# Performance work log

Measured on AMD Instinct MI355X. Metric: run time of the kernel, lower is better.

Reference implementation:

```python
import jax, jax.numpy as jnp
import numpy as np

LMAX, MMAX = 6, 2
C, COUT = 64, 64
E = 50000


def _perms():
    # l-primary coefficient order: for l in 0..lmax, m in -min(l,mmax)..min(l,mmax)
    lp = [(l, m) for l in range(LMAX + 1) for m in range(-min(l, MMAX), min(l, MMAX) + 1)]
    # m-primary order: m=0 block, then for each m>0: real (+m) block then imag (-m) block
    mp = [(l, 0) for l in range(LMAX + 1)]
    for m in range(1, MMAX + 1):
        mp += [(l, m) for l in range(m, LMAX + 1)]
        mp += [(l, -m) for l in range(m, LMAX + 1)]
    to_m = np.array([lp.index(p) for p in mp])   # gather: l-primary -> m-primary
    from_m = np.argsort(to_m)                    # inverse gather: m-primary -> l-primary
    return to_m, from_m

TO_M, FROM_M = _perms()


def setup_inputs() -> dict:
    key = jax.random.key(0)
    ks = jax.random.split(key, 6)
    sz0 = LMAX + 1                      # m_size[0] = 7
    in0 = sz0 * C                       # fc_m0 in_features = 448
    out0 = COUT * sz0                   # fc_m0 out_features = 448
    sz1, sz2 = LMAX, LMAX - 1           # m_size[1]=6, m_size[2]=5
    inp = {
        "x_embedding": jax.random.normal(ks[0], (E, len(TO_M), C), dtype=jnp.float32),
        "x_edge": jax.random.normal(ks[1], (E, 1), dtype=jnp.float32),
        "W0": jax.random.normal(ks[2], (out0, in0), dtype=jnp.float32) / np.sqrt(in0),
        "b0": jnp.zeros((out0,), dtype=jnp.float32),
        "W1": jax.random.normal(ks[3], (2 * COUT * sz1, sz1 * C), dtype=jnp.float32) / np.sqrt(2 * sz1 * C),
        "W2": jax.random.normal(ks[4], (2 * COUT * sz2, sz2 * C), dtype=jnp.float32) / np.sqrt(2 * sz2 * C),
    }
    return inp


def reference(x_embedding, x_edge, W0, b0, W1, W2):
    num_edges = x_embedding.shape[0]
    # _m_primary: permute coefficients to m-primary layout
    x = x_embedding[:, TO_M, :]                         # [E, 29, C]
    out = []
    # m = 0 path (fc_m0 with bias)
    sz0 = LMAX + 1
    x0 = x[:, :sz0, :].reshape(num_edges, sz0 * C)
    x0 = x0 @ W0.T + b0                                 # [E, sz0*COUT]
    out.append(x0.reshape(num_edges, sz0, COUT))
    # m = 1..mmax: SO2_m_Convolution (complex multiply structure)
    offset = sz0
    for m, Wm in zip(range(1, MMAX + 1), (W1, W2)):
        sz = LMAX - m + 1
        xm = x[:, offset:offset + 2 * sz, :].reshape(num_edges, 2, sz * C)
        y = jnp.einsum('enk,ok->eno', xm, Wm)           # [E, 2, 2*sz*COUT]
        half = sz * COUT
        x_r, x_i = y[..., :half], y[..., half:]
        x_m_r = x_r[:, 0:1] - x_i[:, 1:2]
        x_m_i = x_r[:, 1:2] + x_i[:, 0:1]
        xm_out = jnp.concatenate((x_m_r, x_m_i), axis=1)  # [E, 2, sz*COUT]
        out.append(xm_out.reshape(num_edges, 2 * sz, COUT))
        offset += 2 * sz
    out = jnp.concatenate(out, axis=1)                  # [E, 29, COUT] m-primary
    # _l_primary: back to l-primary layout
    return out[:, FROM_M, :]
```

## Files before the change

kernel.cpp:

```cpp
#include <hip/hip_runtime.h>
#include <hip/hip_bf16.h>

typedef __attribute__((ext_vector_type(8))) short short8;
typedef __attribute__((ext_vector_type(4))) float f32x4;
typedef __attribute__((ext_vector_type(4))) unsigned int uint4v;

#define NROW 29
#define CCH 64
#define XSTRIDE 1856
#define N0SQ (448*448)
#define N1SQ (768*768)
#define N2SQ (640*640)

__constant__ int d_TO_M[29] = {0,2,6,11,16,21,26, 3,7,12,17,22,27, 1,5,10,15,20,25,
                               8,13,18,23,28, 4,9,14,19,24};

__device__ __forceinline__ short f2bf(float f) {
    __hip_bfloat16 h = __float2bfloat16(f);
    return __builtin_bit_cast(short, h);
}

__global__ __launch_bounds__(256) void prep_weights(const float* __restrict__ W0,
                                                    const float* __restrict__ W1,
                                                    const float* __restrict__ W2,
                                                    short* __restrict__ ws) {
    int idx = blockIdx.x * 256 + threadIdx.x;
    if (idx < N0SQ) {
        ws[idx] = f2bf(W0[idx]);
        return;
    }
    idx -= N0SQ;
    if (idx < N1SQ) {
        int n = idx / 768, k = idx % 768;
        int no = n / 384, ni = n % 384;
        int ko = k / 384, ki = k % 384;
        float v;
        if (no == ko)      v =  W1[ni * 384 + ki];
        else if (no == 0)  v = -W1[(384 + ni) * 384 + ki];
        else               v =  W1[(384 + ni) * 384 + ki];
        ws[N0SQ + idx] = f2bf(v);
        return;
    }
    idx -= N1SQ;
    if (idx < N2SQ) {
        int n = idx / 640, k = idx % 640;
        int no = n / 320, ni = n % 320;
        int ko = k / 320, ki = k % 320;
        float v;
        if (no == ko)      v =  W2[ni * 320 + ki];
        else if (no == 0)  v = -W2[(320 + ni) * 320 + ki];
        else               v =  W2[(320 + ni) * 320 + ki];
        ws[N0SQ + N1SQ + idx] = f2bf(v);
    }
}

#define LDS_STRIDE 72

__global__ __launch_bounds__(256) void so2_gemm(const float* __restrict__ x,
                                                const float* __restrict__ b0,
                                                const short* __restrict__ wsW,
                                                float* __restrict__ out,
                                                int E, int nwg) {
    int orig = blockIdx.x;
    int q = nwg >> 3, r = nwg & 7;
    int xcd = orig & 7, pos = orig >> 3;
    int wgid = (xcd < r ? xcd * (q + 1) : r * (q + 1) + (xcd - r) * q) + pos;

    int etile = wgid / 15;
    int ncol  = wgid % 15;

    int blk, ntl;
    if (ncol < 4)       { blk = 0; ntl = ncol; }
    else if (ncol < 10) { blk = 1; ntl = ncol - 4; }
    else                { blk = 2; ntl = ncol - 10; }
    const int Kb     = (blk == 0) ? 448 : (blk == 1) ? 768 : 640;
    const int ksteps = Kb >> 6;
    const int kbase  = (blk == 0) ? 0 : (blk == 1) ? 7 : 19;
    const int nrows  = (blk == 0) ? 7 : (blk == 1) ? 12 : 10;
    const long woff  = (blk == 0) ? 0 : (blk == 1) ? (long)N0SQ : (long)(N0SQ + N1SQ);
    const short* Wb  = wsW + woff;

    __shared__ short Alds[128 * LDS_STRIDE];
    __shared__ short Blds[128 * LDS_STRIDE];

    const int tid  = threadIdx.x;
    const int w    = tid >> 6, lane = tid & 63;
    const int wr   = w >> 1,   wc   = w & 1;
    const int lrow = lane & 15, lk  = lane >> 4;
    const int ebase = etile * 128;

    f32x4 acc[4][4] = {};

    f32x4 a0[4], a1[4];
    uint4v breg[4];

    auto load_regs = [&](int kt) {
        int g = d_TO_M[kbase + kt];
        const float* asrc = x + (size_t)g * CCH;
#pragma unroll
        for (int i = 0; i < 4; ++i) {
            int item = i * 256 + tid;
            int row = item >> 3, ch0 = (item & 7) << 3;
            int e = ebase + row;
            if (e < E) {
                const float* p = asrc + (size_t)e * XSTRIDE + ch0;
                a0[i] = *(const f32x4*)p;
                a1[i] = *(const f32x4*)(p + 4);
            } else {
                a0[i] = f32x4{0.f, 0.f, 0.f, 0.f};
                a1[i] = f32x4{0.f, 0.f, 0.f, 0.f};
            }
        }
        const short* bsrc = Wb + kt * 64;
#pragma unroll
        for (int i = 0; i < 4; ++i) {
            int item = i * 256 + tid;
            int row = item >> 3, k0 = (item & 7) << 3;
            int n = ntl * 128 + row;
            if (n < Kb) {
                breg[i] = *(const uint4v*)(bsrc + (size_t)n * Kb + k0);
            } else {
                breg[i] = uint4v{0u, 0u, 0u, 0u};
            }
        }
    };

    auto write_lds = [&]() {
#pragma unroll
        for (int i = 0; i < 4; ++i) {
            int item = i * 256 + tid;
            int row = item >> 3, ch0 = (item & 7) << 3;
            short8 hv;
#pragma unroll
            for (int j = 0; j < 4; ++j) hv[j]     = f2bf(a0[i][j]);
#pragma unroll
            for (int j = 0; j < 4; ++j) hv[4 + j] = f2bf(a1[i][j]);
            *(short8*)&Alds[row * LDS_STRIDE + ch0] = hv;
        }
#pragma unroll
        for (int i = 0; i < 4; ++i) {
            int item = i * 256 + tid;
            int row = item >> 3, k0 = (item & 7) << 3;
            *(uint4v*)&Blds[row * LDS_STRIDE + k0] = breg[i];
        }
    };

    load_regs(0);
    for (int kt = 0; kt < ksteps; ++kt) {
        __syncthreads();
        write_lds();
        if (kt + 1 < ksteps) load_regs(kt + 1);
        __syncthreads();
#pragma unroll
        for (int ks = 0; ks < 2; ++ks) {
            short8 af[4], bf[4];
#pragma unroll
            for (int mf = 0; mf < 4; ++mf)
                af[mf] = *(short8*)&Alds[(wr * 64 + mf * 16 + lrow) * LDS_STRIDE + ks * 32 + lk * 8];
#pragma unroll
            for (int nf = 0; nf < 4; ++nf)
                bf[nf] = *(short8*)&Blds[(wc * 64 + nf * 16 + lrow) * LDS_STRIDE + ks * 32 + lk * 8];
#pragma unroll
            for (int mf = 0; mf < 4; ++mf)
#pragma unroll
                for (int nf = 0; nf < 4; ++nf)
                    acc[mf][nf] = __builtin_amdgcn_mfma_f32_16x16x32_bf16(af[mf], bf[nf], acc[mf][nf], 0, 0, 0);
        }
    }

    int mrow_l = ntl * 2 + wc;
    if (mrow_l < nrows) {
        int lp = d_TO_M[kbase + mrow_l];
        float* op = out + (size_t)lp * CCH;
#pragma unroll
        for (int nf = 0; nf < 4; ++nf) {
            int c = nf * 16 + lrow;
            float bias = 0.f;
            if (blk == 0) bias = b0[mrow_l * 64 + c];
#pragma unroll
            for (int mf = 0; mf < 4; ++mf) {
                int e0 = ebase + wr * 64 + mf * 16 + lk * 4;
#pragma unroll
                for (int j = 0; j < 4; ++j) {
                    int e = e0 + j;
                    if (e < E) op[(size_t)e * XSTRIDE + c] = acc[mf][nf][j] + bias;
                }
            }
        }
    }
}

extern "C" void kernel_launch(void* const* d_in, const int* in_sizes, int n_in,
                              void* d_out, int out_size, void* d_ws, size_t ws_size,
                              hipStream_t stream) {
    const float* x_emb = (const float*)d_in[0];
    const float* W0 = (const float*)d_in[2];
    const float* b0 = (const float*)d_in[3];
    const float* W1 = (const float*)d_in[4];
    const float* W2 = (const float*)d_in[5];
    float* out = (float*)d_out;
    short* ws  = (short*)d_ws;

    const int E = in_sizes[0] / (NROW * CCH);

    const int prep_total = N0SQ + N1SQ + N2SQ;
    prep_weights<<<(prep_total + 255) / 256, 256, 0, stream>>>(W0, W1, W2, ws);

    const int etiles = (E + 127) / 128;
    const int nwg = etiles * 15;
    so2_gemm<<<nwg, 256, 0, stream>>>(x_emb, b0, (const short*)ws, out, E, nwg);
}
```

Before: 370.4 us.

## Double-buffer LDS with 32-wide K tiles and deeper register prefetch

The GEMM main loop moves from a single 64-wide K tile in padded LDS to two 32-wide LDS buffers. Activation loads are prefetched two steps ahead, so global loads, bf16 conversion and LDS writes for the next tile overlap with MFMA work on the current buffer. Load addressing is simplified by precomputing per-thread row pointers and bounds flags. The unpadded 32-short LDS row stride may cause bank conflicts on fragment reads, and the smaller K tile doubles the number of barriers per K.

```diff
diff --git a/kernel.cpp b/kernel.cpp
--- a/kernel.cpp
+++ b/kernel.cpp
@@ -54,34 +54,31 @@
     }
 }
 
-#define LDS_STRIDE 72
-
 __global__ __launch_bounds__(256) void so2_gemm(const float* __restrict__ x,
                                                 const float* __restrict__ b0,
                                                 const short* __restrict__ wsW,
                                                 float* __restrict__ out,
                                                 int E, int nwg) {
     int orig = blockIdx.x;
-    int q = nwg >> 3, r = nwg & 7;
+    int q8 = nwg >> 3, r8 = nwg & 7;
     int xcd = orig & 7, pos = orig >> 3;
-    int wgid = (xcd < r ? xcd * (q + 1) : r * (q + 1) + (xcd - r) * q) + pos;
+    int wgid = (xcd < r8 ? xcd * (q8 + 1) : r8 * (q8 + 1) + (xcd - r8) * q8) + pos;
 
     int etile = wgid / 15;
     int ncol  = wgid % 15;
-
     int blk, ntl;
     if (ncol < 4)       { blk = 0; ntl = ncol; }
     else if (ncol < 10) { blk = 1; ntl = ncol - 4; }
     else                { blk = 2; ntl = ncol - 10; }
     const int Kb     = (blk == 0) ? 448 : (blk == 1) ? 768 : 640;
-    const int ksteps = Kb >> 6;
+    const int ksteps = Kb >> 5;
     const int kbase  = (blk == 0) ? 0 : (blk == 1) ? 7 : 19;
     const int nrows  = (blk == 0) ? 7 : (blk == 1) ? 12 : 10;
     const long woff  = (blk == 0) ? 0 : (blk == 1) ? (long)N0SQ : (long)(N0SQ + N1SQ);
     const short* Wb  = wsW + woff;
 
-    __shared__ short Alds[128 * LDS_STRIDE];
-    __shared__ short Blds[128 * LDS_STRIDE];
+    __shared__ short Alds[2][128 * 32];
+    __shared__ short Blds[2][128 * 32];
 
     const int tid  = threadIdx.x;
     const int w    = tid >> 6, lane = tid & 63;
@@ -89,83 +86,86 @@
     const int lrow = lane & 15, lk  = lane >> 4;
     const int ebase = etile * 128;
 
+    const int qr = tid >> 2;
+    const int rq = tid & 3;
+
+    const int e1 = ebase + qr,      e2 = ebase + 64 + qr;
+    const bool eok1 = e1 < E,       eok2 = e2 < E;
+    const int n1 = ntl * 128 + qr,  n2 = n1 + 64;
+    const bool nok1 = n1 < Kb,      nok2 = n2 < Kb;
+
+    const float* xb1 = x + (size_t)e1 * XSTRIDE + rq * 8;
+    const float* xb2 = x + (size_t)e2 * XSTRIDE + rq * 8;
+    const short* wb1 = Wb + (size_t)n1 * Kb + rq * 8;
+    const short* wb2 = Wb + (size_t)n2 * Kb + rq * 8;
+
     f32x4 acc[4][4] = {};
 
-    f32x4 a0[4], a1[4];
-    uint4v breg[4];
-
-    auto load_regs = [&](int kt) {
-        int g = d_TO_M[kbase + kt];
-        const float* asrc = x + (size_t)g * CCH;
-#pragma unroll
-        for (int i = 0; i < 4; ++i) {
-            int item = i * 256 + tid;
-            int row = item >> 3, ch0 = (item & 7) << 3;
-            int e = ebase + row;
-            if (e < E) {
-                const float* p = asrc + (size_t)e * XSTRIDE + ch0;
-                a0[i] = *(const f32x4*)p;
-                a1[i] = *(const f32x4*)(p + 4);
-            } else {
-                a0[i] = f32x4{0.f, 0.f, 0.f, 0.f};
-                a1[i] = f32x4{0.f, 0.f, 0.f, 0.f};
-            }
-        }
-        const short* bsrc = Wb + kt * 64;
-#pragma unroll
-        for (int i = 0; i < 4; ++i) {
-            int item = i * 256 + tid;
-            int row = item >> 3, k0 = (item & 7) << 3;
-            int n = ntl * 128 + row;
-            if (n < Kb) {
-                breg[i] = *(const uint4v*)(bsrc + (size_t)n * Kb + k0);
-            } else {
-                breg[i] = uint4v{0u, 0u, 0u, 0u};
-            }
-        }
-    };
-
-    auto write_lds = [&]() {
-#pragma unroll
-        for (int i = 0; i < 4; ++i) {
-            int item = i * 256 + tid;
-            int row = item >> 3, ch0 = (item & 7) << 3;
-            short8 hv;
-#pragma unroll
-            for (int j = 0; j < 4; ++j) hv[j]     = f2bf(a0[i][j]);
-#pragma unroll
-            for (int j = 0; j < 4; ++j) hv[4 + j] = f2bf(a1[i][j]);
-            *(short8*)&Alds[row * LDS_STRIDE + ch0] = hv;
-        }
-#pragma unroll
-        for (int i = 0; i < 4; ++i) {
-            int item = i * 256 + tid;
-            int row = item >> 3, k0 = (item & 7) << 3;
-            *(uint4v*)&Blds[row * LDS_STRIDE + k0] = breg[i];
-        }
-    };
-
-    load_regs(0);
-    for (int kt = 0; kt < ksteps; ++kt) {
+    f32x4 sA0[4], sA1[4];
+    uint4v sB[2];
+
+    auto issueA = [&](int kt, f32x4* ar) {
+        int g = d_TO_M[kbase + (kt >> 1)];
+        size_t off = (size_t)g * CCH + (size_t)((kt & 1) * 32);
+        if (eok1) { ar[0] = *(const f32x4*)(xb1 + off); ar[1] = *(const f32x4*)(xb1 + off + 4); }
+        else      { ar[0] = f32x4{0,0,0,0};             ar[1] = f32x4{0,0,0,0}; }
+        if (eok2) { ar[2] = *(const f32x4*)(xb2 + off); ar[3] = *(const f32x4*)(xb2 + off + 4); }
+        else      { ar[2] = f32x4{0,0,0,0};             ar[3] = f32x4{0,0,0,0}; }
+    };
+    auto issueB = [&](int kt) {
+        int off = kt * 32;
+        sB[0] = nok1 ? *(const uint4v*)(wb1 + off) : uint4v{0,0,0,0};
+        sB[1] = nok2 ? *(const uint4v*)(wb2 + off) : uint4v{0,0,0,0};
+    };
+    auto writeL = [&](int pb, const f32x4* ar) {
+        short8 h0, h1;
+#pragma unroll
+        for (int j = 0; j < 4; ++j) {
+            h0[j]     = f2bf(ar[0][j]);  h0[4 + j] = f2bf(ar[1][j]);
+            h1[j]     = f2bf(ar[2][j]);  h1[4 + j] = f2bf(ar[3][j]);
+        }
+        *(short8*)&Alds[pb][qr * 32 + rq * 8]        = h0;
+        *(short8*)&Alds[pb][(64 + qr) * 32 + rq * 8] = h1;
+        *(uint4v*)&Blds[pb][qr * 32 + rq * 8]        = sB[0];
+        *(uint4v*)&Blds[pb][(64 + qr) * 32 + rq * 8] = sB[1];
+    };
+    auto compute = [&](int pb) {
+        short8 af[4], bf[4];
+#pragma unroll
+        for (int mf = 0; mf < 4; ++mf)
+            af[mf] = *(short8*)&Alds[pb][(wr * 64 + mf * 16 + lrow) * 32 + lk * 8];
+#pragma unroll
+        for (int nf = 0; nf < 4; ++nf)
+            bf[nf] = *(short8*)&Blds[pb][(wc * 64 + nf * 16 + lrow) * 32 + lk * 8];
+#pragma unroll
+        for (int mf = 0; mf < 4; ++mf)
+#pragma unroll
+            for (int nf = 0; nf < 4; ++nf)
+                acc[mf][nf] = __builtin_amdgcn_mfma_f32_16x16x32_bf16(af[mf], bf[nf], acc[mf][nf], 0, 0, 0);
+    };
+
+    issueA(0, sA0); issueB(0);
+    issueA(1, sA1);
+    writeL(0, sA0);
+    issueB(1);
+    issueA(2, sA0);
+    __syncthreads();
+
+    for (int kt = 0; kt < ksteps; kt += 2) {
+        writeL(1, sA1);
+        if (kt + 2 < ksteps) {
+            issueB(kt + 2);
+            issueA(kt + 3, sA1);
+        }
+        compute(0);
         __syncthreads();
-        write_lds();
-        if (kt + 1 < ksteps) load_regs(kt + 1);
+        if (kt + 2 < ksteps) {
+            writeL(0, sA0);
+            issueB(kt + 3);
+            if (kt + 4 < ksteps) issueA(kt + 4, sA0);
+        }
+        compute(1);
         __syncthreads();
-#pragma unroll
-        for (int ks = 0; ks < 2; ++ks) {
-            short8 af[4], bf[4];
-#pragma unroll
-            for (int mf = 0; mf < 4; ++mf)
-                af[mf] = *(short8*)&Alds[(wr * 64 + mf * 16 + lrow) * LDS_STRIDE + ks * 32 + lk * 8];
-#pragma unroll
-            for (int nf = 0; nf < 4; ++nf)
-                bf[nf] = *(short8*)&Blds[(wc * 64 + nf * 16 + lrow) * LDS_STRIDE + ks * 32 + lk * 8];
-#pragma unroll
-            for (int mf = 0; mf < 4; ++mf)
-#pragma unroll
-                for (int nf = 0; nf < 4; ++nf)
-                    acc[mf][nf] = __builtin_amdgcn_mfma_f32_16x16x32_bf16(af[mf], bf[nf], acc[mf][nf], 0, 0, 0);
-        }
     }
 
     int mrow_l = ntl * 2 + wc;
```

Result: slower. 418.3 us (+12.9%).

## Pre-pack activations to bf16 tiles and double-buffer GEMM via direct global-to-LDS loads

Applied to the files above, without the earlier changes.

Adds a pack kernel that converts x to bf16 and lays it out in contiguous per-edge-tile, per-row blocks. The main GEMM now stages A and B with global_load_lds straight into swizzled, double-buffered LDS, so the next k-step's loads overlap the current MFMA work, and it requests two workgroups per CU. It also pads the W0 region so every 128-row B tile stays in bounds without per-row checks. The cost is an extra pass that writes and rereads the bf16 copy of x through workspace, with a fallback to the old single-buffer path when the workspace is too small.

```diff
diff --git a/kernel.cpp b/kernel.cpp
--- a/kernel.cpp
+++ b/kernel.cpp
@@ -5,12 +5,11 @@
 typedef __attribute__((ext_vector_type(4))) float f32x4;
 typedef __attribute__((ext_vector_type(4))) unsigned int uint4v;
 
-#define NROW 29
+#define XSTRIDE 1856
 #define CCH 64
-#define XSTRIDE 1856
-#define N0SQ (448*448)
-#define N1SQ (768*768)
-#define N2SQ (640*640)
+#define OFF1 229376
+#define OFF2 819200
+#define WTOT 1228800
 
 __constant__ int d_TO_M[29] = {0,2,6,11,16,21,26, 3,7,12,17,22,27, 1,5,10,15,20,25,
                                8,13,18,23,28, 4,9,14,19,24};
@@ -18,6 +17,11 @@
 __device__ __forceinline__ short f2bf(float f) {
     __hip_bfloat16 h = __float2bfloat16(f);
     return __builtin_bit_cast(short, h);
+}
+
+__device__ __forceinline__ void load16_lds(const void* g, void* l) {
+    __builtin_amdgcn_global_load_lds((const __attribute__((address_space(1))) unsigned int*)g,
+                                     (__attribute__((address_space(3))) unsigned int*)l, 16, 0, 0);
 }
 
 __global__ __launch_bounds__(256) void prep_weights(const float* __restrict__ W0,
@@ -25,50 +29,71 @@
                                                     const float* __restrict__ W2,
                                                     short* __restrict__ ws) {
     int idx = blockIdx.x * 256 + threadIdx.x;
-    if (idx < N0SQ) {
-        ws[idx] = f2bf(W0[idx]);
+    if (idx < OFF1) {
+        ws[idx] = (idx < 448 * 448) ? f2bf(W0[idx]) : (short)0;
         return;
     }
-    idx -= N0SQ;
-    if (idx < N1SQ) {
-        int n = idx / 768, k = idx % 768;
+    if (idx < OFF2) {
+        int i = idx - OFF1;
+        int n = i / 768, k = i % 768;
         int no = n / 384, ni = n % 384;
-        int ko = k / 384, ki = k % 384;
+        int ki = k % 384;
         float v;
-        if (no == ko)      v =  W1[ni * 384 + ki];
-        else if (no == 0)  v = -W1[(384 + ni) * 384 + ki];
-        else               v =  W1[(384 + ni) * 384 + ki];
-        ws[N0SQ + idx] = f2bf(v);
+        if (no == (k / 384)) v =  W1[ni * 384 + ki];
+        else if (no == 0)    v = -W1[(384 + ni) * 384 + ki];
+        else                 v =  W1[(384 + ni) * 384 + ki];
+        ws[idx] = f2bf(v);
         return;
     }
-    idx -= N1SQ;
-    if (idx < N2SQ) {
-        int n = idx / 640, k = idx % 640;
+    if (idx < WTOT) {
+        int i = idx - OFF2;
+        int n = i / 640, k = i % 640;
         int no = n / 320, ni = n % 320;
-        int ko = k / 320, ki = k % 320;
+        int ki = k % 320;
         float v;
-        if (no == ko)      v =  W2[ni * 320 + ki];
-        else if (no == 0)  v = -W2[(320 + ni) * 320 + ki];
-        else               v =  W2[(320 + ni) * 320 + ki];
-        ws[N0SQ + N1SQ + idx] = f2bf(v);
-    }
-}
-
-#define LDS_STRIDE 72
-
-__global__ __launch_bounds__(256) void so2_gemm(const float* __restrict__ x,
-                                                const float* __restrict__ b0,
-                                                const short* __restrict__ wsW,
-                                                float* __restrict__ out,
-                                                int E, int nwg) {
+        if (no == (k / 320)) v =  W2[ni * 320 + ki];
+        else if (no == 0)    v = -W2[(320 + ni) * 320 + ki];
+        else                 v =  W2[(320 + ni) * 320 + ki];
+        ws[idx] = f2bf(v);
+    }
+}
+
+__global__ __launch_bounds__(256) void pack_x(const float* __restrict__ x,
+                                              short* __restrict__ pA, int E) {
+    int b = blockIdx.x;
+    int etile = b / 29, g = b % 29;
+    int ebase = etile * 128;
+    size_t dst = (size_t)b * (128 * 64);
+#pragma unroll
+    for (int j = 0; j < 4; ++j) {
+        int flat = j * 256 + threadIdx.x;
+        int ei = flat >> 3, ch0 = (flat & 7) * 8;
+        int e = ebase + ei;
+        short8 hv;
+        if (e < E) {
+            const float* p = x + (size_t)e * XSTRIDE + g * 64 + ch0;
+            f32x4 v0 = *(const f32x4*)p, v1 = *(const f32x4*)(p + 4);
+#pragma unroll
+            for (int q = 0; q < 4; ++q) { hv[q] = f2bf(v0[q]); hv[4 + q] = f2bf(v1[q]); }
+        } else {
+            hv = short8{0,0,0,0,0,0,0,0};
+        }
+        *(short8*)&pA[dst + (size_t)ei * 64 + ch0] = hv;
+    }
+}
+
+__global__ __launch_bounds__(256, 2) void so2_gemm_p(const short* __restrict__ pA,
+                                                     const float* __restrict__ b0,
+                                                     const short* __restrict__ wsW,
+                                                     float* __restrict__ out,
+                                                     int E, int nwg) {
     int orig = blockIdx.x;
-    int q = nwg >> 3, r = nwg & 7;
+    int q8 = nwg >> 3, r8 = nwg & 7;
     int xcd = orig & 7, pos = orig >> 3;
-    int wgid = (xcd < r ? xcd * (q + 1) : r * (q + 1) + (xcd - r) * q) + pos;
+    int wgid = (xcd < r8 ? xcd * (q8 + 1) : r8 * (q8 + 1) + (xcd - r8) * q8) + pos;
 
     int etile = wgid / 15;
     int ncol  = wgid % 15;
-
     int blk, ntl;
     if (ncol < 4)       { blk = 0; ntl = ncol; }
     else if (ncol < 10) { blk = 1; ntl = ncol - 4; }
@@ -77,11 +102,12 @@
     const int ksteps = Kb >> 6;
     const int kbase  = (blk == 0) ? 0 : (blk == 1) ? 7 : 19;
     const int nrows  = (blk == 0) ? 7 : (blk == 1) ? 12 : 10;
-    const long woff  = (blk == 0) ? 0 : (blk == 1) ? (long)N0SQ : (long)(N0SQ + N1SQ);
+    const long woff  = (blk == 0) ? 0 : (blk == 1) ? (long)OFF1 : (long)OFF2;
     const short* Wb  = wsW + woff;
-
-    __shared__ short Alds[128 * LDS_STRIDE];
-    __shared__ short Blds[128 * LDS_STRIDE];
+    const int n0 = ntl * 128;
+
+    __shared__ short Alds[2][128 * 64];
+    __shared__ short Blds[2][128 * 64];
 
     const int tid  = threadIdx.x;
     const int w    = tid >> 6, lane = tid & 63;
@@ -89,77 +115,152 @@
     const int lrow = lane & 15, lk  = lane >> 4;
     const int ebase = etile * 128;
 
+    const int lr = lane >> 3;
+    const int cs = (lane & 7) ^ lr;
+
     f32x4 acc[4][4] = {};
 
-    f32x4 a0[4], a1[4];
-    uint4v breg[4];
-
-    auto load_regs = [&](int kt) {
+    auto stageA = [&](int kt, int pb) {
         int g = d_TO_M[kbase + kt];
-        const float* asrc = x + (size_t)g * CCH;
+        const short* src = pA + ((size_t)(etile * 29 + g)) * (128 * 64);
+#pragma unroll
+        for (int j = 0; j < 4; ++j) {
+            int rb = w * 32 + j * 8;
+            load16_lds(src + (size_t)(rb + lr) * 64 + cs * 8,
+                       (char*)&Alds[pb][rb * 64] + lane * 16);
+        }
+    };
+    auto stageB = [&](int kt, int pb) {
+        const short* src = Wb + (size_t)kt * 64;
+#pragma unroll
+        for (int j = 0; j < 4; ++j) {
+            int rb = w * 32 + j * 8;
+            load16_lds(src + (size_t)(n0 + rb + lr) * Kb + cs * 8,
+                       (char*)&Blds[pb][rb * 64] + lane * 16);
+        }
+    };
+    auto compute = [&](int pb) {
+#pragma unroll
+        for (int ks = 0; ks < 2; ++ks) {
+            short8 af[4], bf[4];
+#pragma unroll
+            for (int mf = 0; mf < 4; ++mf) {
+                int row = wr * 64 + mf * 16 + lrow;
+                int s = (ks * 4 + lk) ^ (lrow & 7);
+                af[mf] = *(const short8*)&Alds[pb][row * 64 + s * 8];
+            }
+#pragma unroll
+            for (int nf = 0; nf < 4; ++nf) {
+                int row = wc * 64 + nf * 16 + lrow;
+                int s = (ks * 4 + lk) ^ (lrow & 7);
+                bf[nf] = *(const short8*)&Blds[pb][row * 64 + s * 8];
+            }
+#pragma unroll
+            for (int mf = 0; mf < 4; ++mf)
+#pragma unroll
+                for (int nf = 0; nf < 4; ++nf)
+                    acc[mf][nf] = __builtin_amdgcn_mfma_f32_16x16x32_bf16(af[mf], bf[nf], acc[mf][nf], 0, 0, 0);
+        }
+    };
+
+    stageA(0, 0); stageB(0, 0);
+    asm volatile("s_waitcnt vmcnt(0)" ::: "memory");
+    __builtin_amdgcn_s_barrier();
+    __builtin_amdgcn_sched_barrier(0);
+
+    int pb = 0;
+    for (int kt = 0; kt < ksteps; ++kt, pb ^= 1) {
+        if (kt + 1 < ksteps) { stageA(kt + 1, pb ^ 1); stageB(kt + 1, pb ^ 1); }
+        compute(pb);
+        asm volatile("s_waitcnt vmcnt(0)" ::: "memory");
+        __builtin_amdgcn_s_barrier();
+        __builtin_amdgcn_sched_barrier(0);
+    }
+
+    int mrow_l = ntl * 2 + wc;
+    if (mrow_l < nrows) {
+        int lp = d_TO_M[kbase + mrow_l];
+        float* op = out + (size_t)lp * CCH;
+#pragma unroll
+        for (int nf = 0; nf < 4; ++nf) {
+            int c = nf * 16 + lrow;
+            float bias = 0.f;
+            if (blk == 0) bias = b0[mrow_l * 64 + c];
+#pragma unroll
+            for (int mf = 0; mf < 4; ++mf) {
+                int e0 = ebase + wr * 64 + mf * 16 + lk * 4;
+#pragma unroll
+                for (int j = 0; j < 4; ++j) {
+                    int e = e0 + j;
+                    if (e < E) op[(size_t)e * XSTRIDE + c] = acc[mf][nf][j] + bias;
+                }
+            }
+        }
+    }
+}
+
+__global__ __launch_bounds__(256) void so2_gemm_fb(const float* __restrict__ x,
+                                                   const float* __restrict__ b0,
+                                                   const short* __restrict__ wsW,
+                                                   float* __restrict__ out,
+                                                   int E, int nwg) {
+    int orig = blockIdx.x;
+    int q8 = nwg >> 3, r8 = nwg & 7;
+    int xcd = orig & 7, pos = orig >> 3;
+    int wgid = (xcd < r8 ? xcd * (q8 + 1) : r8 * (q8 + 1) + (xcd - r8) * q8) + pos;
+    int etile = wgid / 15, ncol = wgid % 15;
+    int blk, ntl;
+    if (ncol < 4)       { blk = 0; ntl = ncol; }
+    else if (ncol < 10) { blk = 1; ntl = ncol - 4; }
+    else                { blk = 2; ntl = ncol - 10; }
+    const int Kb     = (blk == 0) ? 448 : (blk == 1) ? 768 : 640;
+    const int ksteps = Kb >> 6;
+    const int kbase  = (blk == 0) ? 0 : (blk == 1) ? 7 : 19;
+    const int nrows  = (blk == 0) ? 7 : (blk == 1) ? 12 : 10;
+    const long woff  = (blk == 0) ? 0 : (blk == 1) ? (long)OFF1 : (long)OFF2;
+    const short* Wb  = wsW + woff;
+
+    __shared__ short Alds[128 * 72];
+    __shared__ short Blds[128 * 72];
+    const int tid = threadIdx.x;
+    const int w = tid >> 6, lane = tid & 63;
+    const int wr = w >> 1, wc = w & 1;
+    const int lrow = lane & 15, lk = lane >> 4;
+    const int ebase = etile * 128;
+    f32x4 acc[4][4] = {};
+
+    for (int kt = 0; kt < ksteps; ++kt) {
+        int g = d_TO_M[kbase + kt];
+        __syncthreads();
 #pragma unroll
         for (int i = 0; i < 4; ++i) {
             int item = i * 256 + tid;
             int row = item >> 3, ch0 = (item & 7) << 3;
             int e = ebase + row;
+            f32x4 a0{0,0,0,0}, a1{0,0,0,0};
             if (e < E) {
-                const float* p = asrc + (size_t)e * XSTRIDE + ch0;
-                a0[i] = *(const f32x4*)p;
-                a1[i] = *(const f32x4*)(p + 4);
-            } else {
-                a0[i] = f32x4{0.f, 0.f, 0.f, 0.f};
-                a1[i] = f32x4{0.f, 0.f, 0.f, 0.f};
-            }
-        }
-        const short* bsrc = Wb + kt * 64;
-#pragma unroll
-        for (int i = 0; i < 4; ++i) {
-            int item = i * 256 + tid;
-            int row = item >> 3, k0 = (item & 7) << 3;
+                const float* p = x + (size_t)e * XSTRIDE + (size_t)g * CCH + ch0;
+                a0 = *(const f32x4*)p; a1 = *(const f32x4*)(p + 4);
+            }
+            short8 hv;
+#pragma unroll
+            for (int q = 0; q < 4; ++q) { hv[q] = f2bf(a0[q]); hv[4 + q] = f2bf(a1[q]); }
+            *(short8*)&Alds[row * 72 + ch0] = hv;
             int n = ntl * 128 + row;
-            if (n < Kb) {
-                breg[i] = *(const uint4v*)(bsrc + (size_t)n * Kb + k0);
-            } else {
-                breg[i] = uint4v{0u, 0u, 0u, 0u};
-            }
-        }
-    };
-
-    auto write_lds = [&]() {
-#pragma unroll
-        for (int i = 0; i < 4; ++i) {
-            int item = i * 256 + tid;
-            int row = item >> 3, ch0 = (item & 7) << 3;
-            short8 hv;
-#pragma unroll
-            for (int j = 0; j < 4; ++j) hv[j]     = f2bf(a0[i][j]);
-#pragma unroll
-            for (int j = 0; j < 4; ++j) hv[4 + j] = f2bf(a1[i][j]);
-            *(short8*)&Alds[row * LDS_STRIDE + ch0] = hv;
-        }
-#pragma unroll
-        for (int i = 0; i < 4; ++i) {
-            int item = i * 256 + tid;
-            int row = item >> 3, k0 = (item & 7) << 3;
-            *(uint4v*)&Blds[row * LDS_STRIDE + k0] = breg[i];
-        }
-    };
-
-    load_regs(0);
-    for (int kt = 0; kt < ksteps; ++kt) {
-        __syncthreads();
-        write_lds();
-        if (kt + 1 < ksteps) load_regs(kt + 1);
+            uint4v bv = (n < Kb) ? *(const uint4v*)(Wb + (size_t)n * Kb + kt * 64 + ch0)
+                                 : uint4v{0,0,0,0};
+            *(uint4v*)&Blds[row * 72 + ch0] = bv;
+        }
         __syncthreads();
 #pragma unroll
         for (int ks = 0; ks < 2; ++ks) {
             short8 af[4], bf[4];
 #pragma unroll
             for (int mf = 0; mf < 4; ++mf)
-                af[mf] = *(short8*)&Alds[(wr * 64 + mf * 16 + lrow) * LDS_STRIDE + ks * 32 + lk * 8];
+                af[mf] = *(short8*)&Alds[(wr * 64 + mf * 16 + lrow) * 72 + ks * 32 + lk * 8];
 #pragma unroll
             for (int nf = 0; nf < 4; ++nf)
-                bf[nf] = *(short8*)&Blds[(wc * 64 + nf * 16 + lrow) * LDS_STRIDE + ks * 32 + lk * 8];
+                bf[nf] = *(short8*)&Blds[(wc * 64 + nf * 16 + lrow) * 72 + ks * 32 + lk * 8];
 #pragma unroll
             for (int mf = 0; mf < 4; ++mf)
 #pragma unroll
@@ -175,8 +276,7 @@
 #pragma unroll
         for (int nf = 0; nf < 4; ++nf) {
             int c = nf * 16 + lrow;
-            float bias = 0.f;
-            if (blk == 0) bias = b0[mrow_l * 64 + c];
+            float bias = (blk == 0) ? b0[mrow_l * 64 + c] : 0.f;
 #pragma unroll
             for (int mf = 0; mf < 4; ++mf) {
                 int e0 = ebase + wr * 64 + mf * 16 + lk * 4;
@@ -201,12 +301,20 @@
     float* out = (float*)d_out;
     short* ws  = (short*)d_ws;
 
-    const int E = in_sizes[0] / (NROW * CCH);
-
-    const int prep_total = N0SQ + N1SQ + N2SQ;
-    prep_weights<<<(prep_total + 255) / 256, 256, 0, stream>>>(W0, W1, W2, ws);
-
+    const int E = in_sizes[0] / (29 * CCH);
     const int etiles = (E + 127) / 128;
     const int nwg = etiles * 15;
-    so2_gemm<<<nwg, 256, 0, stream>>>(x_emb, b0, (const short*)ws, out, E, nwg);
-}
+
+    prep_weights<<<(WTOT + 255) / 256, 256, 0, stream>>>(W0, W1, W2, ws);
+
+    const size_t packA_elems = (size_t)etiles * 29 * 128 * 64;
+    const size_t need_bytes = ((size_t)WTOT + packA_elems) * sizeof(short);
+
+    if (ws_size >= need_bytes) {
+        short* pA = ws + WTOT;
+        pack_x<<<etiles * 29, 256, 0, stream>>>(x_emb, pA, E);
+        so2_gemm_p<<<nwg, 256, 0, stream>>>(pA, b0, (const short*)ws, out, E, nwg);
+    } else {
+        so2_gemm_fb<<<nwg, 256, 0, stream>>>(x_emb, b0, (const short*)ws, out, E, nwg);
+    }
+}
```

New measurement: 456.6 us. 23.3% more time.
